# Kernel tuning notes

Measured on AMD Instinct MI355X. Metric: run time of the kernel, lower is better.

The kernel has to match this reference:

```python
import jax, jax.numpy as jnp
import numpy as np
import math

DEPTH = 3
RATIO = 0.5
EPS = 1e-5


def _mlp_ln(h, W1, b1, W2, b2, W3, b3, g, beta):
    h = jax.nn.gelu(h @ W1 + b1, approximate=False)
    h = jax.nn.gelu(h @ W2 + b2, approximate=False)
    h = h @ W3 + b3
    mu = jnp.mean(h, axis=-1, keepdims=True)
    var = jnp.mean((h - mu) ** 2, axis=-1, keepdims=True)
    return g * (h - mu) * jax.lax.rsqrt(var + EPS) + beta


def _node_to_node(x, s, r, n, p):
    # two-way gather -> scatter_add -> MLP+LN. Row n of x_pad is a zero dummy
    # node that absorbs edges dropped by pooling (fixed-size, jit-friendly).
    x_pad = jnp.concatenate([x, jnp.zeros((1, x.shape[1]), x.dtype)], axis=0)
    msg = x_pad[jnp.concatenate([s, r])]            # [2E, C]
    recv = jnp.concatenate([r, s])                  # [2E]
    agg = jax.ops.segment_sum(msg, recv, num_segments=n + 1)[:n]
    return _mlp_ln(agg, *p)


def _forward(x, senders, receivers, pool_w, down_p, up_p):
    s, r = senders, receivers
    xs, edges, perms = [x], [(s, r)], []
    n = x.shape[0]
    for i in range(DEPTH):
        k = math.ceil(RATIO * n)  # PyG topk: ceil(ratio * N)
        w = pool_w[i]
        score = jnp.tanh(x @ w / jnp.linalg.norm(w))
        vals, perm = jax.lax.top_k(score, k)
        x = x[perm] * vals[:, None]
        # remap edges; dropped nodes (and old dummy n) map to new dummy k
        nmap = jnp.full((n + 1,), k, dtype=s.dtype).at[perm].set(
            jnp.arange(k, dtype=s.dtype))
        ns_, nr_ = nmap[s], nmap[r]
        invalid = (ns_ == k) | (nr_ == k)
        s = jnp.where(invalid, k, ns_)
        r = jnp.where(invalid, k, nr_)
        x = _node_to_node(x, s, r, k, down_p[i])
        if i < DEPTH - 1:
            xs.append(x)
            edges.append((s, r))
        perms.append(perm)
        n = k
    for i in range(DEPTH):
        j = DEPTH - 1 - i
        res = xs[j]
        s, r = edges[j]
        perm = perms[j]
        up = jnp.zeros_like(res).at[perm].set(x)
        x = jnp.concatenate([res, up], axis=-1)  # sum_res=False -> concat
        x = _node_to_node(x, s, r, res.shape[0], up_p[i])
    return x


def setup_inputs() -> dict:
    key = jax.random.key(0)
    ks = jax.random.split(key, 16)
    N, E, C, D = 50000, 600000, 128, DEPTH
    f32 = jnp.float32

    def lin(k, fi, fo):
        return (jax.random.normal(k, (D, fi, fo), f32) / np.sqrt(fi)).astype(f32)

    return {
        'x': jax.random.normal(ks[0], (N, C), f32),
        'senders': jax.random.randint(ks[1], (E,), 0, N, dtype=jnp.int32),
        'receivers': jax.random.randint(ks[2], (E,), 0, N, dtype=jnp.int32),
        'pool_w': jax.random.normal(ks[3], (D, C), f32),
        'down_W1': lin(ks[4], C, C), 'down_b1': jnp.zeros((D, C), f32),
        'down_W2': lin(ks[5], C, C), 'down_b2': jnp.zeros((D, C), f32),
        'down_W3': lin(ks[6], C, C), 'down_b3': jnp.zeros((D, C), f32),
        'down_g': jnp.ones((D, C), f32), 'down_beta': jnp.zeros((D, C), f32),
        'up_W1': lin(ks[7], 2 * C, C), 'up_b1': jnp.zeros((D, C), f32),
        'up_W2': lin(ks[8], C, C), 'up_b2': jnp.zeros((D, C), f32),
        'up_W3': lin(ks[9], C, C), 'up_b3': jnp.zeros((D, C), f32),
        'up_g': jnp.ones((D, C), f32), 'up_beta': jnp.zeros((D, C), f32),
    }


def reference(x, senders, receivers, pool_w,
              down_W1, down_b1, down_W2, down_b2, down_W3, down_b3,
              down_g, down_beta,
              up_W1, up_b1, up_W2, up_b2, up_W3, up_b3, up_g, up_beta):
    down_p = [(down_W1[i], down_b1[i], down_W2[i], down_b2[i],
               down_W3[i], down_b3[i], down_g[i], down_beta[i])
              for i in range(DEPTH)]
    up_p = [(up_W1[i], up_b1[i], up_W2[i], up_b2[i],
             up_W3[i], up_b3[i], up_g[i], up_beta[i])
            for i in range(DEPTH)]
    return _forward(x, senders, receivers, pool_w, down_p, up_p)
```

## Files before the change

### kernel.cpp

```cpp
#include <hip/hip_runtime.h>
#include <math.h>


typedef unsigned short u16;
typedef short bf16x8 __attribute__((ext_vector_type(8)));
typedef float f32x4 __attribute__((ext_vector_type(4)));

__device__ __forceinline__ unsigned int fkey(float f) {
  unsigned int b = __float_as_uint(f);
  return (b & 0x80000000u) ? ~b : (b | 0x80000000u);
}

__device__ __forceinline__ float gelu_f(float v) {
  return 0.5f * v * (1.0f + erff(v * 0.70710678118654752f));
}

__device__ __forceinline__ u16 f2bf(float f) {
  unsigned u = __float_as_uint(f);
  u = (u + 0x7FFFu + ((u >> 16) & 1u)) >> 16;
  return (u16)u;
}
__device__ __forceinline__ float bf2f(u16 u) {
  return __uint_as_float(((unsigned)u) << 16);
}

__global__ void score_kernel(const float* __restrict__ x, const float* __restrict__ w,
                             float* __restrict__ key, float* __restrict__ valt, int n) {
  int wave = threadIdx.x >> 6, lane = threadIdx.x & 63;
  int i = blockIdx.x * 4 + wave;
  if (i >= n) return;
  float2 xv = *(const float2*)&x[(size_t)i * 128 + lane * 2];
  float2 wv = *(const float2*)&w[lane * 2];
  double d  = (double)xv.x * wv.x + (double)xv.y * wv.y;
  double nw = (double)wv.x * wv.x + (double)wv.y * wv.y;
  for (int o = 32; o; o >>= 1) { d += __shfl_down(d, o, 64); nw += __shfl_down(nw, o, 64); }
  if (lane == 0) {
    key[i]  = (float)d;
    valt[i] = (float)tanh(d / sqrt(nw));
  }
}

__global__ void preamble_kernel(const float* __restrict__ x, u16* __restrict__ xb, int n,
                                const float* __restrict__ uW1, const float* __restrict__ uW2,
                                const float* __restrict__ uW3, u16* __restrict__ wt1,
                                u16* __restrict__ wt2, u16* __restrict__ wt3,
                                const float* __restrict__ poolw, double* __restrict__ sqn,
                                u16* __restrict__ z0, u16* __restrict__ z1,
                                u16* __restrict__ z2, int nbX) {
  int b = blockIdx.x;
  if (b < nbX) {
    int gid = b * 256 + threadIdx.x;
    if (gid < n * 32) {
      float4 a = *(const float4*)&x[(size_t)gid * 4];
      *(ushort4*)&xb[(size_t)gid * 4] =
          make_ushort4(f2bf(a.x), f2bf(a.y), f2bf(a.z), f2bf(a.w));
    }
    return;
  }
  b -= nbX;
  if (b < 768) {
    int i = b * 256 + threadIdx.x;
    int lvl = i >> 16, rem = i & 65535;
    if (rem < 32768) {
      int k = rem >> 7, c = rem & 127;
      wt1[(size_t)lvl * 32768 + c * 256 + k] = f2bf(uW1[(size_t)lvl * 32768 + rem]);
    } else if (rem < 49152) {
      int j = rem - 32768; int k = j >> 7, c = j & 127;
      wt2[(size_t)lvl * 16384 + c * 128 + k] = f2bf(uW2[(size_t)lvl * 16384 + j]);
    } else {
      int j = rem - 49152; int k = j >> 7, c = j & 127;
      wt3[(size_t)lvl * 16384 + c * 128 + k] = f2bf(uW3[(size_t)lvl * 16384 + j]);
    }
    return;
  }
  b -= 768;
  if (b == 0) {
    if (threadIdx.x < 64) {
      int lane = threadIdx.x;
      for (int l = 0; l < 3; ++l) {
        float2 wv = *(const float2*)&poolw[l * 128 + lane * 2];
        double nw = (double)wv.x * wv.x + (double)wv.y * wv.y;
        for (int o = 32; o; o >>= 1) nw += __shfl_down(nw, o, 64);
        if (lane == 0) sqn[l] = sqrt(nw);
      }
    }
    return;
  }
  int t = threadIdx.x;
  if (t < 128) { z0[t] = 0; z1[t] = 0; z2[t] = 0; }
}

__global__ void hist_hi_kernel(const float* __restrict__ key, int* __restrict__ hist,
                               int* __restrict__ csum, int n) {
  __shared__ int lc[256];
  lc[threadIdx.x] = 0;
  __syncthreads();
  int i = blockIdx.x * 256 + threadIdx.x;
  if (i < n) {
    unsigned b = fkey(key[i]) >> 16;
    atomicAdd(&hist[b], 1);
    atomicAdd(&lc[b >> 8], 1);
  }
  __syncthreads();
  int v = lc[threadIdx.x];
  if (v) atomicAdd(&csum[threadIdx.x], v);
}

__global__ void hist_lo_kernel(const float* __restrict__ key, const int* __restrict__ meta,
                               int* __restrict__ hist, int* __restrict__ csum, int n) {
  __shared__ int lc[256];
  lc[threadIdx.x] = 0;
  __syncthreads();
  int i = blockIdx.x * 256 + threadIdx.x;
  if (i < n) {
    unsigned u = fkey(key[i]);
    if ((u >> 16) == (unsigned)meta[0]) {
      unsigned b = u & 0xFFFFu;
      atomicAdd(&hist[b], 1);
      atomicAdd(&lc[b >> 8], 1);
    }
  }
  __syncthreads();
  int v = lc[threadIdx.x];
  if (v) atomicAdd(&csum[threadIdx.x], v);
}

__global__ void find_hi2_kernel(const int* __restrict__ hist, const int* __restrict__ csum,
                                int* __restrict__ meta, int k) {
  __shared__ int s[256];
  __shared__ int cSh, cumSh;
  int t = threadIdx.x;
  s[t] = csum[t];
  __syncthreads();
  if (t == 0) {
    int cum = 0, c = 0;
    for (int i = 255; i >= 0; --i) {
      if (cum + s[i] >= k) { c = i; break; }
      cum += s[i];
    }
    cSh = c; cumSh = cum;
  }
  __syncthreads();
  int c = cSh;
  s[t] = hist[c * 256 + t];
  __syncthreads();
  if (t == 0) {
    int cum = cumSh;
    for (int b = 255; b >= 0; --b) {
      int v = s[b];
      if (cum + v >= k) { meta[0] = c * 256 + b; meta[1] = k - cum; break; }
      cum += v;
    }
  }
}

__global__ void find_lo2_kernel(const int* __restrict__ hist, const int* __restrict__ csum,
                                int* __restrict__ meta) {
  __shared__ int s[256];
  __shared__ int cSh, cumSh;
  int t = threadIdx.x;
  int m = meta[1], B = meta[0];
  s[t] = csum[t];
  __syncthreads();
  if (t == 0) {
    int cum = 0, c = 0;
    for (int i = 255; i >= 0; --i) {
      if (cum + s[i] >= m) { c = i; break; }
      cum += s[i];
    }
    cSh = c; cumSh = cum;
  }
  __syncthreads();
  int c = cSh;
  s[t] = hist[c * 256 + t];
  __syncthreads();
  if (t == 0) {
    int cum = cumSh;
    for (int b = 255; b >= 0; --b) {
      int v = s[b];
      if (cum + v >= m) {
        meta[3] = (int)((((unsigned)B) << 16) | (unsigned)(c * 256 + b));
        meta[4] = m - cum;
        break;
      }
      cum += v;
    }
    meta[5] = 0;
  }
}

__global__ void tie_count_kernel(const float* __restrict__ key, const int* __restrict__ meta,
                                 int* __restrict__ tcnt, int n) {
  __shared__ int cnt[4];
  unsigned uT = (unsigned)meta[3];
  int i = blockIdx.x * 256 + threadIdx.x;
  bool tie = (i < n) && (fkey(key[i]) == uT);
  unsigned long long m = __ballot(tie);
  int lane = threadIdx.x & 63, w = threadIdx.x >> 6;
  if (lane == 0) cnt[w] = __popcll(m);
  __syncthreads();
  if (threadIdx.x == 0) tcnt[blockIdx.x] = cnt[0] + cnt[1] + cnt[2] + cnt[3];
}

__global__ void tie_mark_kernel(const float* __restrict__ key, const int* __restrict__ meta,
                                const int* __restrict__ tcnt, unsigned char* __restrict__ selt,
                                int n) {
  __shared__ int red[256];
  __shared__ int woff[4];
  int t = threadIdx.x;
  red[t] = (t < (int)blockIdx.x) ? tcnt[t] : 0;
  __syncthreads();
  for (int s = 128; s; s >>= 1) {
    if (t < s) red[t] += red[t + s];
    __syncthreads();
  }
  int blockbase = red[0];
  unsigned uT = (unsigned)meta[3];
  int tsel = meta[4];
  int i = blockIdx.x * 256 + t;
  bool tie = (i < n) && (fkey(key[i]) == uT);
  unsigned long long m = __ballot(tie);
  int lane = t & 63, w = t >> 6;
  if (lane == 0) woff[w] = __popcll(m);
  __syncthreads();
  if (t == 0) {
    int c = 0;
    for (int q = 0; q < 4; ++q) { int v = woff[q]; woff[q] = c; c += v; }
  }
  __syncthreads();
  if (tie) {
    int pre = __popcll(m & ((1ull << lane) - 1ull));
    int rank = blockbase + woff[w] + pre;
    selt[i] = (rank < tsel) ? 1 : 0;
  }
}

__global__ void select_kernel(const float* __restrict__ key, const float* __restrict__ valt,
                              const unsigned char* __restrict__ selt, int* __restrict__ meta,
                              int* __restrict__ perm, float* __restrict__ vals,
                              int* __restrict__ nmap, int n, int k) {
  int i = blockIdx.x * 256 + threadIdx.x;
  if (i > n) return;
  if (i == n) { nmap[n] = k; return; }
  unsigned u  = fkey(key[i]);
  unsigned uT = (unsigned)meta[3];
  bool sel = (u > uT) || (u == uT && selt[i] != 0);
  if (sel) {
    int slot = atomicAdd(&meta[5], 1);
    perm[slot] = i; vals[slot] = valt[i]; nmap[i] = slot;
  } else {
    nmap[i] = k;
  }
}

__global__ void pool_kernel(const float* __restrict__ x, const int* __restrict__ perm,
                            const float* __restrict__ vals, float* __restrict__ xp, int k) {
  int gid = blockIdx.x * 256 + threadIdx.x;
  int t = gid >> 5;
  if (t >= k) return;
  int c = (gid & 31) << 2;
  float v = vals[t];
  float4 a = *(const float4*)&x[(size_t)perm[t] * 128 + c];
  a.x *= v; a.y *= v; a.z *= v; a.w *= v;
  *(float4*)&xp[(size_t)t * 128 + c] = a;
}

__global__ void remap_deg_rank_kernel(const int* __restrict__ s_in, const int* __restrict__ r_in,
                                      const int* __restrict__ nmap, int* __restrict__ s_out,
                                      int* __restrict__ r_out, int* __restrict__ deg,
                                      int* __restrict__ rkS, int* __restrict__ rkR,
                                      int E, int k) {
  int e = blockIdx.x * 256 + threadIdx.x;
  if (e >= E) return;
  int a = nmap[s_in[e]], b = nmap[r_in[e]];
  if (a == k || b == k) { a = k; b = k; }
  s_out[e] = a; r_out[e] = b;
  if (a < k) {
    rkR[e] = atomicAdd(&deg[b], 1);
    rkS[e] = atomicAdd(&deg[a], 1);
  }
}

__global__ void deg_rank_kernel(const int* __restrict__ s, const int* __restrict__ r,
                                int* __restrict__ deg, int* __restrict__ rkS,
                                int* __restrict__ rkR, int E, int n) {
  int e = blockIdx.x * 256 + threadIdx.x;
  if (e >= E) return;
  int ss = s[e];
  if (ss >= n) return;
  int rr = r[e];
  rkR[e] = atomicAdd(&deg[rr], 1);
  rkS[e] = atomicAdd(&deg[ss], 1);
}

__global__ void scan_part_kernel(const int* __restrict__ deg, int* __restrict__ bsum, int n) {
  __shared__ int l[256];
  int i = blockIdx.x * 256 + threadIdx.x;
  l[threadIdx.x] = (i < n) ? deg[i] : 0;
  __syncthreads();
  for (int s = 128; s; s >>= 1) {
    if (threadIdx.x < s) l[threadIdx.x] += l[threadIdx.x + s];
    __syncthreads();
  }
  if (threadIdx.x == 0) bsum[blockIdx.x] = l[0];
}

__global__ void scan_final_kernel(const int* __restrict__ deg, const int* __restrict__ bsum,
                                  int* __restrict__ off, int n) {
  __shared__ int red[256];
  __shared__ int l[256];
  int i = blockIdx.x * 256 + threadIdx.x;
  int t = threadIdx.x;
  red[t] = (t < (int)blockIdx.x) ? bsum[t] : 0;
  __syncthreads();
  for (int s = 128; s; s >>= 1) {
    if (t < s) red[t] += red[t + s];
    __syncthreads();
  }
  int base = red[0];
  int v = (i < n) ? deg[i] : 0;
  l[t] = v;
  __syncthreads();
#pragma unroll
  for (int s = 1; s < 256; s <<= 1) {
    int add = (t >= s) ? l[t - s] : 0;
    __syncthreads();
    l[t] += add;
    __syncthreads();
  }
  int incl = l[t];
  if (i < n) {
    int e = base + incl - v;
    off[i] = e;
    if (i == n - 1) off[n] = base + incl;
  }
}

__global__ void rank_scatter_kernel(const int* __restrict__ s, const int* __restrict__ r,
                                    const int* __restrict__ off, const int* __restrict__ rkS,
                                    const int* __restrict__ rkR, int* __restrict__ idx,
                                    int E, int n) {
  int e = blockIdx.x * 256 + threadIdx.x;
  if (e >= E) return;
  int ss = s[e];
  if (ss >= n) return;
  int rr = r[e];
  idx[off[rr] + rkR[e]] = ss;
  idx[off[ss] + rkS[e]] = rr;
}

__global__ void idxup3_kernel(const int* __restrict__ idxA, const int* __restrict__ nmA,
                              const int* __restrict__ lenA, int* __restrict__ outA,
                              const int* __restrict__ idxB, const int* __restrict__ nmB,
                              const int* __restrict__ lenB, int* __restrict__ outB,
                              const int* __restrict__ idxC, const int* __restrict__ nmC,
                              const int* __restrict__ lenC, int* __restrict__ outC,
                              int nbSeg, int maxlen) {
  int seg = blockIdx.x / nbSeg;
  int j = (blockIdx.x - seg * nbSeg) * 256 + threadIdx.x;
  if (j >= maxlen) return;
  const int* idx; const int* nm; const int* len; int* out;
  if (seg == 0)      { idx = idxA; nm = nmA; len = lenA; out = outA; }
  else if (seg == 1) { idx = idxB; nm = nmB; len = lenB; out = outB; }
  else               { idx = idxC; nm = nmC; len = lenC; out = outC; }
  if (j >= len[0]) return;
  out[j] = nm[idx[j]];
}

__global__ void agg_kernel(const float* __restrict__ x, const int* __restrict__ off,
                           const int* __restrict__ idx, float* __restrict__ agg, int n) {
  int wave = threadIdx.x >> 6, lane = threadIdx.x & 63;
  int v = blockIdx.x * 4 + wave;
  if (v >= n) return;
  int lo = __builtin_amdgcn_readfirstlane(off[v]);
  int hi = __builtin_amdgcn_readfirstlane(off[v + 1]);
  int c = lane * 2;
  float ax = 0.f, ay = 0.f;
  int j = lo;
  for (; j + 4 <= hi; j += 4) {
    int u0 = idx[j], u1 = idx[j + 1], u2 = idx[j + 2], u3 = idx[j + 3];
    float2 a0 = *(const float2*)&x[(size_t)u0 * 128 + c];
    float2 a1 = *(const float2*)&x[(size_t)u1 * 128 + c];
    float2 a2 = *(const float2*)&x[(size_t)u2 * 128 + c];
    float2 a3 = *(const float2*)&x[(size_t)u3 * 128 + c];
    ax += a0.x + a1.x + a2.x + a3.x;
    ay += a0.y + a1.y + a2.y + a3.y;
  }
  for (; j < hi; ++j) {
    int u = idx[j];
    float2 a = *(const float2*)&x[(size_t)u * 128 + c];
    ax += a.x; ay += a.y;
  }
  float2 o; o.x = ax; o.y = ay;
  *(float2*)&agg[(size_t)v * 128 + c] = o;
}

__global__ void agg_up_kernel(const u16* __restrict__ res_bf, const u16* __restrict__ xd_bf,
                              const int* __restrict__ idxR, const int* __restrict__ idxU,
                              const int* __restrict__ off, u16* __restrict__ agg, int n) {
  int wave = threadIdx.x >> 6, lane = threadIdx.x & 63;
  int v = blockIdx.x * 4 + wave;
  if (v >= n) return;
  int lo = __builtin_amdgcn_readfirstlane(off[v]);
  int hi = __builtin_amdgcn_readfirstlane(off[v + 1]);
  int g = lane >> 4, sl = lane & 15;
  bool upH = g >= 2;
  bool second = (g & 1) != 0;
  const u16* bp = (upH ? xd_bf : res_bf) + sl * 8;
  float4 a0 = {0.f, 0.f, 0.f, 0.f}, a1 = {0.f, 0.f, 0.f, 0.f};

#define ACC_ROW(EE)                                     \
  do {                                                  \
    uint4 wq = *(const uint4*)(bp + (size_t)(EE) * 128);\
    a0.x += __uint_as_float(wq.x << 16);                \
    a0.y += __uint_as_float(wq.x & 0xffff0000u);        \
    a0.z += __uint_as_float(wq.y << 16);                \
    a0.w += __uint_as_float(wq.y & 0xffff0000u);        \
    a1.x += __uint_as_float(wq.z << 16);                \
    a1.y += __uint_as_float(wq.z & 0xffff0000u);        \
    a1.z += __uint_as_float(wq.w << 16);                \
    a1.w += __uint_as_float(wq.w & 0xffff0000u);        \
  } while (0)

  int j = lo;
  for (; j + 4 <= hi; j += 4) {
    int er0 = idxR[j], er1 = idxR[j + 1], er2 = idxR[j + 2], er3 = idxR[j + 3];
    int eu0 = idxU[j], eu1 = idxU[j + 1], eu2 = idxU[j + 2], eu3 = idxU[j + 3];
    int eA = upH ? (second ? eu1 : eu0) : (second ? er1 : er0);
    int eB = upH ? (second ? eu3 : eu2) : (second ? er3 : er2);
    ACC_ROW(eA);
    ACC_ROW(eB);
  }
  for (; j + 2 <= hi; j += 2) {
    int er0 = idxR[j], er1 = idxR[j + 1];
    int eu0 = idxU[j], eu1 = idxU[j + 1];
    int e = upH ? (second ? eu1 : eu0) : (second ? er1 : er0);
    ACC_ROW(e);
  }
  if (j < hi) {
    int er = idxR[j], eu = idxU[j];
    int e = upH ? eu : er;
    if (!second) ACC_ROW(e);
  }
#undef ACC_ROW

  a0.x += __shfl_xor(a0.x, 16, 64);
  a0.y += __shfl_xor(a0.y, 16, 64);
  a0.z += __shfl_xor(a0.z, 16, 64);
  a0.w += __shfl_xor(a0.w, 16, 64);
  a1.x += __shfl_xor(a1.x, 16, 64);
  a1.y += __shfl_xor(a1.y, 16, 64);
  a1.z += __shfl_xor(a1.z, 16, 64);
  a1.w += __shfl_xor(a1.w, 16, 64);

  if (!second) {
    bf16x8 ov;
    ov[0] = (short)f2bf(a0.x); ov[1] = (short)f2bf(a0.y);
    ov[2] = (short)f2bf(a0.z); ov[3] = (short)f2bf(a0.w);
    ov[4] = (short)f2bf(a1.x); ov[5] = (short)f2bf(a1.y);
    ov[6] = (short)f2bf(a1.z); ov[7] = (short)f2bf(a1.w);
    *(bf16x8*)&agg[(size_t)v * 256 + (upH ? 128 : 0) + sl * 8] = ov;
  }
}

template <bool GELU>
__global__ __launch_bounds__(256) void gemm_kernel(const float* __restrict__ A,
                                                   const float* __restrict__ W,
                                                   const float* __restrict__ bias,
                                                   float* __restrict__ out, int n) {
  __shared__ float As[32 * 32];
  __shared__ float Ws[32 * 128];
  int t = threadIdx.x;
  int row0 = blockIdx.x * 32;
  int colg = (t & 31) << 2;
  int rowg = (t >> 5) << 2;
  float acc[4][4];
#pragma unroll
  for (int i = 0; i < 4; ++i)
#pragma unroll
    for (int j = 0; j < 4; ++j) acc[i][j] = 0.f;

  for (int k0 = 0; k0 < 128; k0 += 32) {
    __syncthreads();
    {
      int ar = t >> 3, ac = (t & 7) << 2;
      float4 av = make_float4(0.f, 0.f, 0.f, 0.f);
      if (row0 + ar < n) av = *(const float4*)&A[(size_t)(row0 + ar) * 128 + k0 + ac];
      *(float4*)&As[ar * 32 + ac] = av;
    }
#pragma unroll
    for (int l = 0; l < 4; ++l) {
      int id = t + l * 256;
      int kk = id >> 5, wc = (id & 31) << 2;
      *(float4*)&Ws[kk * 128 + wc] = *(const float4*)&W[(size_t)(k0 + kk) * 128 + wc];
    }
    __syncthreads();
#pragma unroll
    for (int kk = 0; kk < 32; kk += 4) {
      float4 wv[4];
#pragma unroll
      for (int j = 0; j < 4; ++j) wv[j] = *(const float4*)&Ws[(kk + j) * 128 + colg];
#pragma unroll
      for (int i = 0; i < 4; ++i) {
        float4 av = *(const float4*)&As[(rowg + i) * 32 + kk];
        acc[i][0] += av.x * wv[0].x + av.y * wv[1].x + av.z * wv[2].x + av.w * wv[3].x;
        acc[i][1] += av.x * wv[0].y + av.y * wv[1].y + av.z * wv[2].y + av.w * wv[3].y;
        acc[i][2] += av.x * wv[0].z + av.y * wv[1].z + av.z * wv[2].z + av.w * wv[3].z;
        acc[i][3] += av.x * wv[0].w + av.y * wv[1].w + av.z * wv[2].w + av.w * wv[3].w;
      }
    }
  }
  float4 bv = *(const float4*)&bias[colg];
#pragma unroll
  for (int i = 0; i < 4; ++i) {
    int rr = row0 + rowg + i;
    if (rr < n) {
      float4 o = make_float4(acc[i][0] + bv.x, acc[i][1] + bv.y, acc[i][2] + bv.z, acc[i][3] + bv.w);
      if (GELU) { o.x = gelu_f(o.x); o.y = gelu_f(o.y); o.z = gelu_f(o.z); o.w = gelu_f(o.w); }
      *(float4*)&out[(size_t)rr * 128 + colg] = o;
    }
  }
}

template <int K>
__global__ __launch_bounds__(256) void gemm_mfma_kernel(const u16* __restrict__ A,
                                                        const u16* __restrict__ WT,
                                                        const float* __restrict__ bias,
                                                        u16* __restrict__ out, int n) {
  __shared__ u16 As[64 * 72];
  __shared__ u16 Ws[128 * 72];
  int t = threadIdx.x;
  int lane = t & 63, wave = t >> 6;
  int row0 = blockIdx.x * 64;
  f32x4 acc[8];
#pragma unroll
  for (int i = 0; i < 8; ++i) acc[i] = (f32x4){0.f, 0.f, 0.f, 0.f};

  for (int k0 = 0; k0 < K; k0 += 64) {
    __syncthreads();
#pragma unroll
    for (int i = 0; i < 2; ++i) {
      int c = t + i * 256;
      int r = c >> 3, seg = c & 7;
      bf16x8 v = {0, 0, 0, 0, 0, 0, 0, 0};
      if (row0 + r < n) v = *(const bf16x8*)&A[(size_t)(row0 + r) * K + k0 + seg * 8];
      *(bf16x8*)&As[r * 72 + seg * 8] = v;
    }
#pragma unroll
    for (int i = 0; i < 4; ++i) {
      int c = t + i * 256;
      int r = c >> 3, seg = c & 7;
      *(bf16x8*)&Ws[r * 72 + seg * 8] = *(const bf16x8*)&WT[(size_t)r * K + k0 + seg * 8];
    }
    __syncthreads();
#pragma unroll
    for (int kk = 0; kk < 64; kk += 32) {
      bf16x8 a = *(const bf16x8*)&As[(wave * 16 + (lane & 15)) * 72 + kk + (lane >> 4) * 8];
#pragma unroll
      for (int ct = 0; ct < 8; ++ct) {
        bf16x8 b = *(const bf16x8*)&Ws[(ct * 16 + (lane & 15)) * 72 + kk + (lane >> 4) * 8];
        acc[ct] = __builtin_amdgcn_mfma_f32_16x16x32_bf16(a, b, acc[ct], 0, 0, 0);
      }
    }
  }
  int colb = lane & 15, rquad = lane >> 4;
#pragma unroll
  for (int ct = 0; ct < 8; ++ct) {
#pragma unroll
    for (int r = 0; r < 4; ++r) {
      int row = row0 + wave * 16 + rquad * 4 + r;
      if (row < n) {
        int col = ct * 16 + colb;
        out[(size_t)row * 128 + col] = f2bf(gelu_f(acc[ct][r] + bias[col]));
      }
    }
  }
}

template <bool WF32, bool WBF>
__global__ __launch_bounds__(256) void gemm_mfma_ln_kernel(
    const u16* __restrict__ A, const u16* __restrict__ WT, const float* __restrict__ bias,
    const float* __restrict__ g, const float* __restrict__ beta,
    float* __restrict__ out, u16* __restrict__ outbf, int n) {
  __shared__ u16 As[64 * 72];
  __shared__ u16 Ws[128 * 72];
  int t = threadIdx.x;
  int lane = t & 63, wave = t >> 6;
  int row0 = blockIdx.x * 64;
  f32x4 acc[8];
#pragma unroll
  for (int i = 0; i < 8; ++i) acc[i] = (f32x4){0.f, 0.f, 0.f, 0.f};

  for (int k0 = 0; k0 < 128; k0 += 64) {
    __syncthreads();
#pragma unroll
    for (int i = 0; i < 2; ++i) {
      int c = t + i * 256;
      int r = c >> 3, seg = c & 7;
      bf16x8 v = {0, 0, 0, 0, 0, 0, 0, 0};
      if (row0 + r < n) v = *(const bf16x8*)&A[(size_t)(row0 + r) * 128 + k0 + seg * 8];
      *(bf16x8*)&As[r * 72 + seg * 8] = v;
    }
#pragma unroll
    for (int i = 0; i < 4; ++i) {
      int c = t + i * 256;
      int r = c >> 3, seg = c & 7;
      *(bf16x8*)&Ws[r * 72 + seg * 8] = *(const bf16x8*)&WT[(size_t)r * 128 + k0 + seg * 8];
    }
    __syncthreads();
#pragma unroll
    for (int kk = 0; kk < 64; kk += 32) {
      bf16x8 a = *(const bf16x8*)&As[(wave * 16 + (lane & 15)) * 72 + kk + (lane >> 4) * 8];
#pragma unroll
      for (int ct = 0; ct < 8; ++ct) {
        bf16x8 b = *(const bf16x8*)&Ws[(ct * 16 + (lane & 15)) * 72 + kk + (lane >> 4) * 8];
        acc[ct] = __builtin_amdgcn_mfma_f32_16x16x32_bf16(a, b, acc[ct], 0, 0, 0);
      }
    }
  }
  int colb = lane & 15, rquad = lane >> 4;
  float bv[8], gv[8], bev[8];
#pragma unroll
  for (int ct = 0; ct < 8; ++ct) {
    int col = ct * 16 + colb;
    bv[ct] = bias[col]; gv[ct] = g[col]; bev[ct] = beta[col];
  }
#pragma unroll
  for (int r = 0; r < 4; ++r) {
    float s1 = 0.f;
#pragma unroll
    for (int ct = 0; ct < 8; ++ct) s1 += acc[ct][r] + bv[ct];
#pragma unroll
    for (int o = 1; o <= 8; o <<= 1) s1 += __shfl_xor(s1, o, 64);
    float mu = s1 * (1.0f / 128.0f);
    float s2 = 0.f;
#pragma unroll
    for (int ct = 0; ct < 8; ++ct) { float d = acc[ct][r] + bv[ct] - mu; s2 += d * d; }
#pragma unroll
    for (int o = 1; o <= 8; o <<= 1) s2 += __shfl_xor(s2, o, 64);
    float rs = rsqrtf(s2 * (1.0f / 128.0f) + 1e-5f);
    int row = row0 + wave * 16 + rquad * 4 + r;
    if (row < n) {
#pragma unroll
      for (int ct = 0; ct < 8; ++ct) {
        int col = ct * 16 + colb;
        float o = gv[ct] * (acc[ct][r] + bv[ct] - mu) * rs + bev[ct];
        if (WF32) out[(size_t)row * 128 + col] = o;
        if (WBF)  outbf[(size_t)row * 128 + col] = f2bf(o);
      }
    }
  }
}

template <bool SCORE, bool WBF>
__global__ void ln_kernel(const float* __restrict__ h, const float* __restrict__ g,
                          const float* __restrict__ beta, float* __restrict__ out,
                          u16* __restrict__ outbf, const float* __restrict__ wnext,
                          const double* __restrict__ sqn, float* __restrict__ key,
                          float* __restrict__ valt, int n) {
  int wave = threadIdx.x >> 6, lane = threadIdx.x & 63;
  int i = blockIdx.x * 4 + wave;
  if (i >= n) return;
  float2 hv = *(const float2*)&h[(size_t)i * 128 + lane * 2];
  float s = hv.x + hv.y;
  for (int o = 32; o; o >>= 1) s += __shfl_down(s, o, 64);
  float mu = __shfl(s, 0, 64) * (1.0f / 128.0f);
  float dx = hv.x - mu, dy = hv.y - mu;
  float q = dx * dx + dy * dy;
  for (int o = 32; o; o >>= 1) q += __shfl_down(q, o, 64);
  float var = __shfl(q, 0, 64) * (1.0f / 128.0f);
  float rs = rsqrtf(var + 1e-5f);
  float2 gv = *(const float2*)&g[lane * 2];
  float2 bv = *(const float2*)&beta[lane * 2];
  float2 o2; o2.x = gv.x * dx * rs + bv.x; o2.y = gv.y * dy * rs + bv.y;
  *(float2*)&out[(size_t)i * 128 + lane * 2] = o2;
  if (WBF)
    *(ushort2*)&outbf[(size_t)i * 128 + lane * 2] = make_ushort2(f2bf(o2.x), f2bf(o2.y));
  if (SCORE) {
    float2 wv = *(const float2*)&wnext[lane * 2];
    double d = (double)o2.x * wv.x + (double)o2.y * wv.y;
    for (int o = 32; o; o >>= 1) d += __shfl_down(d, o, 64);
    if (lane == 0) {
      key[i]  = (float)d;
      valt[i] = (float)tanh(d / sqn[0]);
    }
  }
}


static inline int cdiv(int a, int b) { return (a + b - 1) / b; }

extern "C" void kernel_launch(void* const* d_in, const int* in_sizes, int n_in,
                              void* d_out, int out_size, void* d_ws, size_t ws_size,
                              hipStream_t stream) {
  const float* x0   = (const float*)d_in[0];
  const int*   snd  = (const int*)d_in[1];
  const int*   rcv  = (const int*)d_in[2];
  const float* poolw = (const float*)d_in[3];
  const float* dW1 = (const float*)d_in[4];
  const float* db1 = (const float*)d_in[5];
  const float* dW2 = (const float*)d_in[6];
  const float* db2 = (const float*)d_in[7];
  const float* dW3 = (const float*)d_in[8];
  const float* db3 = (const float*)d_in[9];
  const float* dg  = (const float*)d_in[10];
  const float* dbe = (const float*)d_in[11];
  const float* uW1 = (const float*)d_in[12];
  const float* ub1 = (const float*)d_in[13];
  const float* uW2 = (const float*)d_in[14];
  const float* ub2 = (const float*)d_in[15];
  const float* uW3 = (const float*)d_in[16];
  const float* ub3 = (const float*)d_in[17];
  const float* ug  = (const float*)d_in[18];
  const float* ube = (const float*)d_in[19];

  const int N0 = in_sizes[0] / 128;
  const int E  = in_sizes[1];
  const int N1 = (N0 + 1) / 2, N2 = (N1 + 1) / 2, N3 = (N2 + 1) / 2;

  char* p = (char*)d_ws;
  auto alloc = [&](size_t bytes) -> void* {
    void* r = (void*)p;
    p += (bytes + 255) & ~(size_t)255;
    return r;
  };
  float* key  = (float*)alloc((size_t)N0 * 4);
  float* valt = (float*)alloc((size_t)N0 * 4);
  int*   hist = (int*)alloc((size_t)(2 * 65536 + 512) * 4);
  int*   csum_hi = hist + 2 * 65536;
  int*   csum_lo = hist + 2 * 65536 + 256;
  int*   meta = (int*)alloc(64 * 4);
  int*   tcnt = (int*)alloc(512 * 4);
  int*   bsum = (int*)alloc(256 * 4);
  unsigned char* selt = (unsigned char*)alloc((size_t)N0);
  int*   nm1 = (int*)alloc((size_t)(N0 + 1) * 4);
  int*   nm2 = (int*)alloc((size_t)(N1 + 1) * 4);
  int*   nm3 = (int*)alloc((size_t)(N2 + 1) * 4);
  int*   perm0 = (int*)alloc((size_t)N1 * 4);
  int*   perm1 = (int*)alloc((size_t)N2 * 4);
  int*   perm2 = (int*)alloc((size_t)N3 * 4);
  float* vals  = (float*)alloc((size_t)N1 * 4);
  double* sqn  = (double*)alloc(8 * 8);
  int* s1 = (int*)alloc((size_t)E * 4); int* r1 = (int*)alloc((size_t)E * 4);
  int* s2 = (int*)alloc((size_t)E * 4); int* r2 = (int*)alloc((size_t)E * 4);
  int* s3 = (int*)alloc((size_t)E * 4); int* r3 = (int*)alloc((size_t)E * 4);
  float* x1 = (float*)alloc((size_t)N1 * 128 * 4);
  float* x2 = (float*)alloc((size_t)N2 * 128 * 4);
  float* x3 = (float*)alloc((size_t)N3 * 128 * 4);
  float* xp = (float*)alloc((size_t)N1 * 128 * 4);
  float* aggf = (float*)alloc((size_t)N1 * 128 * 4);
  float* h1f  = (float*)alloc((size_t)N1 * 128 * 4);
  float* h2f  = (float*)alloc((size_t)N1 * 128 * 4);
  u16* agg_bf = (u16*)alloc((size_t)N0 * 256 * 2);
  u16* res0_bf = (u16*)alloc((size_t)N0 * 128 * 2);
  u16* res1_bf = (u16*)alloc((size_t)N1 * 128 * 2);
  u16* res2_bf = (u16*)alloc((size_t)N2 * 128 * 2);
  u16* x3_bf   = (u16*)alloc((size_t)(N3 + 1) * 128 * 2);
  u16* xu2_bf  = (u16*)alloc((size_t)(N2 + 1) * 128 * 2);
  u16* xu1_bf  = (u16*)alloc((size_t)(N1 + 1) * 128 * 2);
  u16* wt1 = (u16*)alloc((size_t)3 * 128 * 256 * 2);
  u16* wt2 = (u16*)alloc((size_t)3 * 128 * 128 * 2);
  u16* wt3 = (u16*)alloc((size_t)3 * 128 * 128 * 2);
  int* off0 = (int*)alloc((size_t)(N0 + 1) * 4); int* deg0 = (int*)alloc((size_t)N0 * 4);
  int* idx0 = (int*)alloc((size_t)2 * E * 4);
  int* off1 = (int*)alloc((size_t)(N1 + 1) * 4); int* deg1 = (int*)alloc((size_t)N1 * 4);
  int* idx1 = (int*)alloc((size_t)2 * E * 4);
  int* off2 = (int*)alloc((size_t)(N2 + 1) * 4); int* deg2 = (int*)alloc((size_t)N2 * 4);
  int* idx2 = (int*)alloc((size_t)2 * E * 4);
  int* off3 = (int*)alloc((size_t)(N3 + 1) * 4); int* deg3 = (int*)alloc((size_t)N3 * 4);
  int* idx3 = (int*)alloc((size_t)2 * E * 4);
  int* idxu0 = (int*)alloc((size_t)2 * E * 4);
  int* idxu1 = (int*)alloc((size_t)2 * E * 4);
  int* idxu2 = (int*)alloc((size_t)2 * E * 4);

  u16* h1b = (u16*)xp;
  u16* h2b = (u16*)s1;
  int* rkS = (int*)agg_bf;
  int* rkR = rkS + E;

  auto run_scan = [&](int* degB, int* offB, int n) {
    int nb = cdiv(n, 256);
    scan_part_kernel<<<nb, 256, 0, stream>>>(degB, bsum, n);
    scan_final_kernel<<<nb, 256, 0, stream>>>(degB, bsum, offB, n);
  };

  {
    int nbX = cdiv(N0 * 32, 256);
    preamble_kernel<<<nbX + 768 + 2, 256, 0, stream>>>(
        x0, res0_bf, N0, uW1, uW2, uW3, wt1, wt2, wt3, poolw, sqn,
        x3_bf + (size_t)N3 * 128, xu2_bf + (size_t)N2 * 128,
        xu1_bf + (size_t)N1 * 128, nbX);
  }

  hipMemsetAsync(deg0, 0, (size_t)N0 * 4, stream);
  deg_rank_kernel<<<cdiv(E, 256), 256, 0, stream>>>(snd, rcv, deg0, rkS, rkR, E, N0);
  run_scan(deg0, off0, N0);
  rank_scatter_kernel<<<cdiv(E, 256), 256, 0, stream>>>(snd, rcv, off0, rkS, rkR, idx0, E, N0);

  auto down_step = [&](int n, int k, const float* xcur, const int* sin, const int* rin,
                       int* sout, int* rout, int* permL, int* nmL, float* xnext,
                       u16* xnext_bf, int lvl, int* offL, int* degL, int* idxL) {
    int nb = cdiv(n, 256);
    hipMemsetAsync(hist, 0, (size_t)(2 * 65536 + 512) * 4, stream);
    hist_hi_kernel<<<nb, 256, 0, stream>>>(key, hist, csum_hi, n);
    find_hi2_kernel<<<1, 256, 0, stream>>>(hist, csum_hi, meta, k);
    hist_lo_kernel<<<nb, 256, 0, stream>>>(key, meta, hist + 65536, csum_lo, n);
    find_lo2_kernel<<<1, 256, 0, stream>>>(hist + 65536, csum_lo, meta);
    tie_count_kernel<<<nb, 256, 0, stream>>>(key, meta, tcnt, n);
    tie_mark_kernel<<<nb, 256, 0, stream>>>(key, meta, tcnt, selt, n);
    select_kernel<<<cdiv(n + 1, 256), 256, 0, stream>>>(key, valt, selt, meta, permL, vals, nmL, n, k);
    pool_kernel<<<cdiv(k * 32, 256), 256, 0, stream>>>(xcur, permL, vals, xp, k);
    hipMemsetAsync(degL, 0, (size_t)k * 4, stream);
    remap_deg_rank_kernel<<<cdiv(E, 256), 256, 0, stream>>>(
        sin, rin, nmL, sout, rout, degL, rkS, rkR, E, k);
    run_scan(degL, offL, k);
    rank_scatter_kernel<<<cdiv(E, 256), 256, 0, stream>>>(sout, rout, offL, rkS, rkR, idxL, E, k);
    agg_kernel<<<cdiv(k, 4), 256, 0, stream>>>(xp, offL, idxL, aggf, k);
    gemm_kernel<true><<<cdiv(k, 32), 256, 0, stream>>>(
        aggf, dW1 + (size_t)lvl * 128 * 128, db1 + (size_t)lvl * 128, h1f, k);
    gemm_kernel<true><<<cdiv(k, 32), 256, 0, stream>>>(
        h1f, dW2 + (size_t)lvl * 128 * 128, db2 + (size_t)lvl * 128, h2f, k);
    gemm_kernel<false><<<cdiv(k, 32), 256, 0, stream>>>(
        h2f, dW3 + (size_t)lvl * 128 * 128, db3 + (size_t)lvl * 128, h1f, k);
    if (lvl < 2)
      ln_kernel<true, true><<<cdiv(k, 4), 256, 0, stream>>>(
          h1f, dg + (size_t)lvl * 128, dbe + (size_t)lvl * 128, xnext, xnext_bf,
          poolw + (size_t)(lvl + 1) * 128, sqn + (lvl + 1), key, valt, k);
    else
      ln_kernel<false, true><<<cdiv(k, 4), 256, 0, stream>>>(
          h1f, dg + (size_t)lvl * 128, dbe + (size_t)lvl * 128, xnext, xnext_bf,
          nullptr, nullptr, nullptr, nullptr, k);
  };

  score_kernel<<<cdiv(N0, 4), 256, 0, stream>>>(x0, poolw, key, valt, N0);
  down_step(N0, N1, x0, snd, rcv, s1, r1, perm0, nm1, x1, res1_bf, 0, off1, deg1, idx1);
  down_step(N1, N2, x1, s1, r1, s2, r2, perm1, nm2, x2, res2_bf, 1, off2, deg2, idx2);
  down_step(N2, N3, x2, s2, r2, s3, r3, perm2, nm3, x3, x3_bf, 2, off3, deg3, idx3);

  {
    int nbSeg = cdiv(2 * E, 256);
    idxup3_kernel<<<3 * nbSeg, 256, 0, stream>>>(
        idx2, nm3, off2 + N2, idxu2,
        idx1, nm2, off1 + N1, idxu1,
        idx0, nm1, off0 + N0, idxu0, nbSeg, 2 * E);
  }

  auto up_step = [&](int n, const u16* resb, const u16* xdb, int lvl,
                     const int* offL, const int* idxL, const int* idxUL,
                     bool wantF32, float* outF32, u16* outBF) {
    agg_up_kernel<<<cdiv(n, 4), 256, 0, stream>>>(resb, xdb, idxL, idxUL, offL, agg_bf, n);
    gemm_mfma_kernel<256><<<cdiv(n, 64), 256, 0, stream>>>(
        agg_bf, wt1 + (size_t)lvl * 128 * 256, ub1 + (size_t)lvl * 128, h1b, n);
    gemm_mfma_kernel<128><<<cdiv(n, 64), 256, 0, stream>>>(
        h1b, wt2 + (size_t)lvl * 128 * 128, ub2 + (size_t)lvl * 128, h2b, n);
    if (wantF32)
      gemm_mfma_ln_kernel<true, false><<<cdiv(n, 64), 256, 0, stream>>>(
          h2b, wt3 + (size_t)lvl * 128 * 128, ub3 + (size_t)lvl * 128,
          ug + (size_t)lvl * 128, ube + (size_t)lvl * 128, outF32, nullptr, n);
    else
      gemm_mfma_ln_kernel<false, true><<<cdiv(n, 64), 256, 0, stream>>>(
          h2b, wt3 + (size_t)lvl * 128 * 128, ub3 + (size_t)lvl * 128,
          ug + (size_t)lvl * 128, ube + (size_t)lvl * 128, nullptr, outBF, n);
  };

  up_step(N2, res2_bf, x3_bf,  0, off2, idx2, idxu2, false, nullptr, xu2_bf);
  up_step(N1, res1_bf, xu2_bf, 1, off1, idx1, idxu1, false, nullptr, xu1_bf);
  up_step(N0, res0_bf, xu1_bf, 2, off0, idx0, idxu0, true, (float*)d_out, nullptr);

  (void)n_in; (void)out_size; (void)ws_size;
}
```

Before: 923.1 us.

## Store residual and unpooled features in combined 256-wide bf16 rows with scatter-on-write

Residual and upsampled features now share one bf16 table per level, 256 columns wide. The residual fills the first half and the unpooled coarse output is scattered by perm into the second half when it is produced. The separate idxup remap kernel and the second index array go away, so each up-aggregation gathers one contiguous 512-byte row per edge with a single index. The down-path float aggregation also switches to float4 loads with the two half-waves handling alternate edges. The trade-off is scattered, uncoalesced writes in the LN and GEMM epilogues, plus extra zero-fill of the upper halves.

After: 1.028 ms. 11.4% more time.

```diff
diff --git a/kernel.cpp b/kernel.cpp
--- a/kernel.cpp
+++ b/kernel.cpp
@@ -40,20 +40,21 @@
   }
 }
 
-__global__ void preamble_kernel(const float* __restrict__ x, u16* __restrict__ xb, int n,
+__global__ void preamble_kernel(const float* __restrict__ x, u16* __restrict__ c0, int n,
                                 const float* __restrict__ uW1, const float* __restrict__ uW2,
                                 const float* __restrict__ uW3, u16* __restrict__ wt1,
                                 u16* __restrict__ wt2, u16* __restrict__ wt3,
                                 const float* __restrict__ poolw, double* __restrict__ sqn,
-                                u16* __restrict__ z0, u16* __restrict__ z1,
-                                u16* __restrict__ z2, int nbX) {
+                                int nbX) {
   int b = blockIdx.x;
   if (b < nbX) {
     int gid = b * 256 + threadIdx.x;
     if (gid < n * 32) {
+      int row = gid >> 5, q = gid & 31;
       float4 a = *(const float4*)&x[(size_t)gid * 4];
-      *(ushort4*)&xb[(size_t)gid * 4] =
+      *(ushort4*)&c0[(size_t)row * 256 + q * 4] =
           make_ushort4(f2bf(a.x), f2bf(a.y), f2bf(a.z), f2bf(a.w));
+      *(ushort4*)&c0[(size_t)row * 256 + 128 + q * 4] = make_ushort4(0, 0, 0, 0);
     }
     return;
   }
@@ -84,10 +85,7 @@
         if (lane == 0) sqn[l] = sqrt(nw);
       }
     }
-    return;
-  }
-  int t = threadIdx.x;
-  if (t < 128) { z0[t] = 0; z1[t] = 0; z2[t] = 0; }
+  }
 }
 
 __global__ void hist_hi_kernel(const float* __restrict__ key, int* __restrict__ hist,
@@ -349,24 +347,6 @@
   idx[off[ss] + rkS[e]] = rr;
 }
 
-__global__ void idxup3_kernel(const int* __restrict__ idxA, const int* __restrict__ nmA,
-                              const int* __restrict__ lenA, int* __restrict__ outA,
-                              const int* __restrict__ idxB, const int* __restrict__ nmB,
-                              const int* __restrict__ lenB, int* __restrict__ outB,
-                              const int* __restrict__ idxC, const int* __restrict__ nmC,
-                              const int* __restrict__ lenC, int* __restrict__ outC,
-                              int nbSeg, int maxlen) {
-  int seg = blockIdx.x / nbSeg;
-  int j = (blockIdx.x - seg * nbSeg) * 256 + threadIdx.x;
-  if (j >= maxlen) return;
-  const int* idx; const int* nm; const int* len; int* out;
-  if (seg == 0)      { idx = idxA; nm = nmA; len = lenA; out = outA; }
-  else if (seg == 1) { idx = idxB; nm = nmB; len = lenB; out = outB; }
-  else               { idx = idxC; nm = nmC; len = lenC; out = outC; }
-  if (j >= len[0]) return;
-  out[j] = nm[idx[j]];
-}
-
 __global__ void agg_kernel(const float* __restrict__ x, const int* __restrict__ off,
                            const int* __restrict__ idx, float* __restrict__ agg, int n) {
   int wave = threadIdx.x >> 6, lane = threadIdx.x & 63;
@@ -374,44 +354,53 @@
   if (v >= n) return;
   int lo = __builtin_amdgcn_readfirstlane(off[v]);
   int hi = __builtin_amdgcn_readfirstlane(off[v + 1]);
-  int c = lane * 2;
-  float ax = 0.f, ay = 0.f;
+  int g = lane >> 5, sl = lane & 31;
+  const float* bp = x + sl * 4;
+  float4 acc = {0.f, 0.f, 0.f, 0.f};
+#define ACC_F(EE)                                        \
+  do {                                                   \
+    float4 w_ = *(const float4*)(bp + (size_t)(EE) * 128);\
+    acc.x += w_.x; acc.y += w_.y; acc.z += w_.z; acc.w += w_.w; \
+  } while (0)
   int j = lo;
-  for (; j + 4 <= hi; j += 4) {
-    int u0 = idx[j], u1 = idx[j + 1], u2 = idx[j + 2], u3 = idx[j + 3];
-    float2 a0 = *(const float2*)&x[(size_t)u0 * 128 + c];
-    float2 a1 = *(const float2*)&x[(size_t)u1 * 128 + c];
-    float2 a2 = *(const float2*)&x[(size_t)u2 * 128 + c];
-    float2 a3 = *(const float2*)&x[(size_t)u3 * 128 + c];
-    ax += a0.x + a1.x + a2.x + a3.x;
-    ay += a0.y + a1.y + a2.y + a3.y;
-  }
-  for (; j < hi; ++j) {
-    int u = idx[j];
-    float2 a = *(const float2*)&x[(size_t)u * 128 + c];
-    ax += a.x; ay += a.y;
-  }
-  float2 o; o.x = ax; o.y = ay;
-  *(float2*)&agg[(size_t)v * 128 + c] = o;
-}
-
-__global__ void agg_up_kernel(const u16* __restrict__ res_bf, const u16* __restrict__ xd_bf,
-                              const int* __restrict__ idxR, const int* __restrict__ idxU,
+  for (; j + 8 <= hi; j += 8) {
+    int q0 = idx[j],     q1 = idx[j + 1], q2 = idx[j + 2], q3 = idx[j + 3];
+    int q4 = idx[j + 4], q5 = idx[j + 5], q6 = idx[j + 6], q7 = idx[j + 7];
+    ACC_F(g ? q1 : q0);
+    ACC_F(g ? q3 : q2);
+    ACC_F(g ? q5 : q4);
+    ACC_F(g ? q7 : q6);
+  }
+  for (; j + 2 <= hi; j += 2) {
+    int q0 = idx[j], q1 = idx[j + 1];
+    ACC_F(g ? q1 : q0);
+  }
+  if (j < hi) {
+    int q0 = idx[j];
+    if (!g) ACC_F(q0);
+  }
+#undef ACC_F
+  acc.x += __shfl_xor(acc.x, 32, 64);
+  acc.y += __shfl_xor(acc.y, 32, 64);
+  acc.z += __shfl_xor(acc.z, 32, 64);
+  acc.w += __shfl_xor(acc.w, 32, 64);
+  if (!g) *(float4*)&agg[(size_t)v * 128 + sl * 4] = acc;
+}
+
+__global__ void agg_up_kernel(const u16* __restrict__ c, const int* __restrict__ idx,
                               const int* __restrict__ off, u16* __restrict__ agg, int n) {
   int wave = threadIdx.x >> 6, lane = threadIdx.x & 63;
   int v = blockIdx.x * 4 + wave;
   if (v >= n) return;
   int lo = __builtin_amdgcn_readfirstlane(off[v]);
   int hi = __builtin_amdgcn_readfirstlane(off[v + 1]);
-  int g = lane >> 4, sl = lane & 15;
-  bool upH = g >= 2;
-  bool second = (g & 1) != 0;
-  const u16* bp = (upH ? xd_bf : res_bf) + sl * 8;
+  int g = lane >> 5, sl = lane & 31;
+  const u16* bp = c + sl * 8;
   float4 a0 = {0.f, 0.f, 0.f, 0.f}, a1 = {0.f, 0.f, 0.f, 0.f};
 
 #define ACC_ROW(EE)                                     \
   do {                                                  \
-    uint4 wq = *(const uint4*)(bp + (size_t)(EE) * 128);\
+    uint4 wq = *(const uint4*)(bp + (size_t)(EE) * 256);\
     a0.x += __uint_as_float(wq.x << 16);                \
     a0.y += __uint_as_float(wq.x & 0xffff0000u);        \
     a0.z += __uint_as_float(wq.y << 16);                \
@@ -423,43 +412,47 @@
   } while (0)
 
   int j = lo;
-  for (; j + 4 <= hi; j += 4) {
-    int er0 = idxR[j], er1 = idxR[j + 1], er2 = idxR[j + 2], er3 = idxR[j + 3];
-    int eu0 = idxU[j], eu1 = idxU[j + 1], eu2 = idxU[j + 2], eu3 = idxU[j + 3];
-    int eA = upH ? (second ? eu1 : eu0) : (second ? er1 : er0);
-    int eB = upH ? (second ? eu3 : eu2) : (second ? er3 : er2);
-    ACC_ROW(eA);
-    ACC_ROW(eB);
+  for (; j + 16 <= hi; j += 16) {
+    int q[16];
+#pragma unroll
+    for (int t2 = 0; t2 < 16; ++t2) q[t2] = idx[j + t2];
+#pragma unroll
+    for (int t2 = 0; t2 < 8; ++t2) ACC_ROW(g ? q[2 * t2 + 1] : q[2 * t2]);
+  }
+  for (; j + 8 <= hi; j += 8) {
+    int q0 = idx[j],     q1 = idx[j + 1], q2 = idx[j + 2], q3 = idx[j + 3];
+    int q4 = idx[j + 4], q5 = idx[j + 5], q6 = idx[j + 6], q7 = idx[j + 7];
+    ACC_ROW(g ? q1 : q0);
+    ACC_ROW(g ? q3 : q2);
+    ACC_ROW(g ? q5 : q4);
+    ACC_ROW(g ? q7 : q6);
   }
   for (; j + 2 <= hi; j += 2) {
-    int er0 = idxR[j], er1 = idxR[j + 1];
-    int eu0 = idxU[j], eu1 = idxU[j + 1];
-    int e = upH ? (second ? eu1 : eu0) : (second ? er1 : er0);
-    ACC_ROW(e);
+    int q0 = idx[j], q1 = idx[j + 1];
+    ACC_ROW(g ? q1 : q0);
   }
   if (j < hi) {
-    int er = idxR[j], eu = idxU[j];
-    int e = upH ? eu : er;
-    if (!second) ACC_ROW(e);
+    int q0 = idx[j];
+    if (!g) ACC_ROW(q0);
   }
 #undef ACC_ROW
 
-  a0.x += __shfl_xor(a0.x, 16, 64);
-  a0.y += __shfl_xor(a0.y, 16, 64);
-  a0.z += __shfl_xor(a0.z, 16, 64);
-  a0.w += __shfl_xor(a0.w, 16, 64);
-  a1.x += __shfl_xor(a1.x, 16, 64);
-  a1.y += __shfl_xor(a1.y, 16, 64);
-  a1.z += __shfl_xor(a1.z, 16, 64);
-  a1.w += __shfl_xor(a1.w, 16, 64);
-
-  if (!second) {
+  a0.x += __shfl_xor(a0.x, 32, 64);
+  a0.y += __shfl_xor(a0.y, 32, 64);
+  a0.z += __shfl_xor(a0.z, 32, 64);
+  a0.w += __shfl_xor(a0.w, 32, 64);
+  a1.x += __shfl_xor(a1.x, 32, 64);
+  a1.y += __shfl_xor(a1.y, 32, 64);
+  a1.z += __shfl_xor(a1.z, 32, 64);
+  a1.w += __shfl_xor(a1.w, 32, 64);
+
+  if (!g) {
     bf16x8 ov;
     ov[0] = (short)f2bf(a0.x); ov[1] = (short)f2bf(a0.y);
     ov[2] = (short)f2bf(a0.z); ov[3] = (short)f2bf(a0.w);
     ov[4] = (short)f2bf(a1.x); ov[5] = (short)f2bf(a1.y);
     ov[6] = (short)f2bf(a1.z); ov[7] = (short)f2bf(a1.w);
-    *(bf16x8*)&agg[(size_t)v * 256 + (upH ? 128 : 0) + sl * 8] = ov;
+    *(bf16x8*)&agg[(size_t)v * 256 + sl * 8] = ov;
   }
 }
 
@@ -581,7 +574,7 @@
 __global__ __launch_bounds__(256) void gemm_mfma_ln_kernel(
     const u16* __restrict__ A, const u16* __restrict__ WT, const float* __restrict__ bias,
     const float* __restrict__ g, const float* __restrict__ beta,
-    float* __restrict__ out, u16* __restrict__ outbf, int n) {
+    float* __restrict__ out, u16* __restrict__ outbf, const int* __restrict__ perm, int n) {
   __shared__ u16 As[64 * 72];
   __shared__ u16 Ws[128 * 72];
   int t = threadIdx.x;
@@ -641,21 +634,23 @@
     float rs = rsqrtf(s2 * (1.0f / 128.0f) + 1e-5f);
     int row = row0 + wave * 16 + rquad * 4 + r;
     if (row < n) {
+      int prow = WBF ? perm[row] : 0;
 #pragma unroll
       for (int ct = 0; ct < 8; ++ct) {
         int col = ct * 16 + colb;
         float o = gv[ct] * (acc[ct][r] + bv[ct] - mu) * rs + bev[ct];
         if (WF32) out[(size_t)row * 128 + col] = o;
-        if (WBF)  outbf[(size_t)row * 128 + col] = f2bf(o);
+        if (WBF)  outbf[(size_t)prow * 256 + 128 + col] = f2bf(o);
       }
     }
   }
 }
 
-template <bool SCORE, bool WBF>
+template <bool SCORE, bool SCATTER>
 __global__ void ln_kernel(const float* __restrict__ h, const float* __restrict__ g,
                           const float* __restrict__ beta, float* __restrict__ out,
-                          u16* __restrict__ outbf, const float* __restrict__ wnext,
+                          u16* __restrict__ cdst, const int* __restrict__ perm,
+                          const float* __restrict__ wnext,
                           const double* __restrict__ sqn, float* __restrict__ key,
                           float* __restrict__ valt, int n) {
   int wave = threadIdx.x >> 6, lane = threadIdx.x & 63;
@@ -674,8 +669,14 @@
   float2 bv = *(const float2*)&beta[lane * 2];
   float2 o2; o2.x = gv.x * dx * rs + bv.x; o2.y = gv.y * dy * rs + bv.y;
   *(float2*)&out[(size_t)i * 128 + lane * 2] = o2;
-  if (WBF)
-    *(ushort2*)&outbf[(size_t)i * 128 + lane * 2] = make_ushort2(f2bf(o2.x), f2bf(o2.y));
+  if (!SCATTER) {
+    *(ushort2*)&cdst[(size_t)i * 256 + lane * 2] = make_ushort2(f2bf(o2.x), f2bf(o2.y));
+    *(ushort2*)&cdst[(size_t)i * 256 + 128 + lane * 2] = make_ushort2(0, 0);
+  } else {
+    int prow = perm[i];
+    *(ushort2*)&cdst[(size_t)prow * 256 + 128 + lane * 2] =
+        make_ushort2(f2bf(o2.x), f2bf(o2.y));
+  }
   if (SCORE) {
     float2 wv = *(const float2*)&wnext[lane * 2];
     double d = (double)o2.x * wv.x + (double)o2.y * wv.y;
@@ -752,12 +753,9 @@
   float* h1f  = (float*)alloc((size_t)N1 * 128 * 4);
   float* h2f  = (float*)alloc((size_t)N1 * 128 * 4);
   u16* agg_bf = (u16*)alloc((size_t)N0 * 256 * 2);
-  u16* res0_bf = (u16*)alloc((size_t)N0 * 128 * 2);
-  u16* res1_bf = (u16*)alloc((size_t)N1 * 128 * 2);
-  u16* res2_bf = (u16*)alloc((size_t)N2 * 128 * 2);
-  u16* x3_bf   = (u16*)alloc((size_t)(N3 + 1) * 128 * 2);
-  u16* xu2_bf  = (u16*)alloc((size_t)(N2 + 1) * 128 * 2);
-  u16* xu1_bf  = (u16*)alloc((size_t)(N1 + 1) * 128 * 2);
+  u16* c0 = (u16*)alloc((size_t)N0 * 256 * 2);
+  u16* c1 = (u16*)alloc((size_t)N1 * 256 * 2);
+  u16* c2 = (u16*)alloc((size_t)N2 * 256 * 2);
   u16* wt1 = (u16*)alloc((size_t)3 * 128 * 256 * 2);
   u16* wt2 = (u16*)alloc((size_t)3 * 128 * 128 * 2);
   u16* wt3 = (u16*)alloc((size_t)3 * 128 * 128 * 2);
@@ -769,9 +767,6 @@
   int* idx2 = (int*)alloc((size_t)2 * E * 4);
   int* off3 = (int*)alloc((size_t)(N3 + 1) * 4); int* deg3 = (int*)alloc((size_t)N3 * 4);
   int* idx3 = (int*)alloc((size_t)2 * E * 4);
-  int* idxu0 = (int*)alloc((size_t)2 * E * 4);
-  int* idxu1 = (int*)alloc((size_t)2 * E * 4);
-  int* idxu2 = (int*)alloc((size_t)2 * E * 4);
 
   u16* h1b = (u16*)xp;
   u16* h2b = (u16*)s1;
@@ -786,10 +781,8 @@
 
   {
     int nbX = cdiv(N0 * 32, 256);
-    preamble_kernel<<<nbX + 768 + 2, 256, 0, stream>>>(
-        x0, res0_bf, N0, uW1, uW2, uW3, wt1, wt2, wt3, poolw, sqn,
-        x3_bf + (size_t)N3 * 128, xu2_bf + (size_t)N2 * 128,
-        xu1_bf + (size_t)N1 * 128, nbX);
+    preamble_kernel<<<nbX + 768 + 1, 256, 0, stream>>>(
+        x0, c0, N0, uW1, uW2, uW3, wt1, wt2, wt3, poolw, sqn, nbX);
   }
 
   hipMemsetAsync(deg0, 0, (size_t)N0 * 4, stream);
@@ -799,7 +792,7 @@
 
   auto down_step = [&](int n, int k, const float* xcur, const int* sin, const int* rin,
                        int* sout, int* rout, int* permL, int* nmL, float* xnext,
-                       u16* xnext_bf, int lvl, int* offL, int* degL, int* idxL) {
+                       u16* cdst, int lvl, int* offL, int* degL, int* idxL) {
     int nb = cdiv(n, 256);
     hipMemsetAsync(hist, 0, (size_t)(2 * 65536 + 512) * 4, stream);
     hist_hi_kernel<<<nb, 256, 0, stream>>>(key, hist, csum_hi, n);
@@ -822,33 +815,28 @@
         h1f, dW2 + (size_t)lvl * 128 * 128, db2 + (size_t)lvl * 128, h2f, k);
     gemm_kernel<false><<<cdiv(k, 32), 256, 0, stream>>>(
         h2f, dW3 + (size_t)lvl * 128 * 128, db3 + (size_t)lvl * 128, h1f, k);
-    if (lvl < 2)
-      ln_kernel<true, true><<<cdiv(k, 4), 256, 0, stream>>>(
-          h1f, dg + (size_t)lvl * 128, dbe + (size_t)lvl * 128, xnext, xnext_bf,
+    if (lvl == 0)
+      ln_kernel<true, false><<<cdiv(k, 4), 256, 0, stream>>>(
+          h1f, dg + (size_t)lvl * 128, dbe + (size_t)lvl * 128, xnext, cdst, nullptr,
+          poolw + (size_t)(lvl + 1) * 128, sqn + (lvl + 1), key, valt, k);
+    else if (lvl == 1)
+      ln_kernel<true, false><<<cdiv(k, 4), 256, 0, stream>>>(
+          h1f, dg + (size_t)lvl * 128, dbe + (size_t)lvl * 128, xnext, cdst, nullptr,
           poolw + (size_t)(lvl + 1) * 128, sqn + (lvl + 1), key, valt, k);
     else
       ln_kernel<false, true><<<cdiv(k, 4), 256, 0, stream>>>(
-          h1f, dg + (size_t)lvl * 128, dbe + (size_t)lvl * 128, xnext, xnext_bf,
+          h1f, dg + (size_t)lvl * 128, dbe + (size_t)lvl * 128, xnext, cdst, perm2,
           nullptr, nullptr, nullptr, nullptr, k);
   };
 
   score_kernel<<<cdiv(N0, 4), 256, 0, stream>>>(x0, poolw, key, valt, N0);
-  down_step(N0, N1, x0, snd, rcv, s1, r1, perm0, nm1, x1, res1_bf, 0, off1, deg1, idx1);
-  down_step(N1, N2, x1, s1, r1, s2, r2, perm1, nm2, x2, res2_bf, 1, off2, deg2, idx2);
-  down_step(N2, N3, x2, s2, r2, s3, r3, perm2, nm3, x3, x3_bf, 2, off3, deg3, idx3);
-
-  {
-    int nbSeg = cdiv(2 * E, 256);
-    idxup3_kernel<<<3 * nbSeg, 256, 0, stream>>>(
-        idx2, nm3, off2 + N2, idxu2,
-        idx1, nm2, off1 + N1, idxu1,
-        idx0, nm1, off0 + N0, idxu0, nbSeg, 2 * E);
-  }
-
-  auto up_step = [&](int n, const u16* resb, const u16* xdb, int lvl,
-                     const int* offL, const int* idxL, const int* idxUL,
-                     bool wantF32, float* outF32, u16* outBF) {
-    agg_up_kernel<<<cdiv(n, 4), 256, 0, stream>>>(resb, xdb, idxL, idxUL, offL, agg_bf, n);
+  down_step(N0, N1, x0, snd, rcv, s1, r1, perm0, nm1, x1, c1, 0, off1, deg1, idx1);
+  down_step(N1, N2, x1, s1, r1, s2, r2, perm1, nm2, x2, c2, 1, off2, deg2, idx2);
+  down_step(N2, N3, x2, s2, r2, s3, r3, perm2, nm3, x3, c2, 2, off3, deg3, idx3);
+
+  auto up_step = [&](int n, const u16* ctab, int lvl, const int* offL, const int* idxL,
+                     bool wantF32, float* outF32, u16* cNext, const int* permNext) {
+    agg_up_kernel<<<cdiv(n, 4), 256, 0, stream>>>(ctab, idxL, offL, agg_bf, n);
     gemm_mfma_kernel<256><<<cdiv(n, 64), 256, 0, stream>>>(
         agg_bf, wt1 + (size_t)lvl * 128 * 256, ub1 + (size_t)lvl * 128, h1b, n);
     gemm_mfma_kernel<128><<<cdiv(n, 64), 256, 0, stream>>>(
@@ -856,16 +844,16 @@
     if (wantF32)
       gemm_mfma_ln_kernel<true, false><<<cdiv(n, 64), 256, 0, stream>>>(
           h2b, wt3 + (size_t)lvl * 128 * 128, ub3 + (size_t)lvl * 128,
-          ug + (size_t)lvl * 128, ube + (size_t)lvl * 128, outF32, nullptr, n);
+          ug + (size_t)lvl * 128, ube + (size_t)lvl * 128, outF32, nullptr, nullptr, n);
     else
       gemm_mfma_ln_kernel<false, true><<<cdiv(n, 64), 256, 0, stream>>>(
           h2b, wt3 + (size_t)lvl * 128 * 128, ub3 + (size_t)lvl * 128,
-          ug + (size_t)lvl * 128, ube + (size_t)lvl * 128, nullptr, outBF, n);
+          ug + (size_t)lvl * 128, ube + (size_t)lvl * 128, nullptr, cNext, permNext, n);
   };
 
-  up_step(N2, res2_bf, x3_bf,  0, off2, idx2, idxu2, false, nullptr, xu2_bf);
-  up_step(N1, res1_bf, xu2_bf, 1, off1, idx1, idxu1, false, nullptr, xu1_bf);
-  up_step(N0, res0_bf, xu1_bf, 2, off0, idx0, idxu0, true, (float*)d_out, nullptr);
+  up_step(N2, c2, 0, off2, idx2, false, nullptr, c1, perm1);
+  up_step(N1, c1, 1, off1, idx1, false, nullptr, c0, perm0);
+  up_step(N0, c0, 2, off0, idx0, true, (float*)d_out, nullptr, nullptr);
 
   (void)n_in; (void)out_size; (void)ws_size;
 }
```
